# Performance work log

Hardware: AMD Instinct MI355X
Metric: run time of the kernel (lower is better)

## Reference

```python
import jax, jax.numpy as jnp
import numpy as np

B, CK, H, W = 1, 64, 30, 54
O, CV, M = 3, 512, 32400
TOP_K = 20


def setup_inputs() -> dict:
    key = jax.random.key(0)
    k1, k2, k3 = jax.random.split(key, 3)
    return {
        "qk": jax.random.normal(k1, (B, CK, H, W), dtype=jnp.float32),
        "mem_k": jax.random.normal(k2, (1, CK, M), dtype=jnp.float32),
        "mem_v": jax.random.normal(k3, (O, CV, M), dtype=jnp.float32),
        "top_k": TOP_K,
    }


def _softmax_w_top(aff, top_k):
    # aff: [B, M, Q]; top-k softmax over the memory axis M (dim=1), zeros elsewhere.
    b, m, q = aff.shape
    xt = aff.transpose(0, 2, 1)                      # [B, Q, M] -> top_k over last axis
    vals, idx = jax.lax.top_k(xt, top_k)             # [B, Q, K]
    soft = jax.nn.softmax(vals, axis=-1)             # stable softmax over the K kept entries
    w = jnp.zeros_like(xt).at[
        jnp.arange(b)[:, None, None],
        jnp.arange(q)[None, :, None],
        idx,
    ].set(soft)                                      # scatter back into [B, Q, M]
    return w.transpose(0, 2, 1)                      # [B, M, Q]


def reference(qk, mem_k, mem_v, top_k):
    b, ck, h, w = qk.shape
    q = h * w
    qk2 = qk.reshape(b, ck, q)                       # [B, CK, Q]
    mk = mem_k[0]                                    # [CK, M]
    a_sq = jnp.sum(mk * mk, axis=0)                  # [M]
    ab = jnp.einsum("cm,bcq->bmq", mk, qk2)          # [B, M, Q]
    scale = np.sqrt(ck).astype(np.float32)
    affinity = (2.0 * ab - a_sq[None, :, None]) / scale
    weights = _softmax_w_top(affinity, top_k)        # [B, M, Q] sparse (top_k nonzeros per column)
    readout = jnp.einsum("ocm,bmq->obcq", mem_v, weights)  # [O, B, CV, Q]
    o, _, cv, _ = readout.shape
    return readout.reshape(o, b, cv, h, q // h)      # [O, B, CV, H, W]
```

## Files before the change

### kernel.cpp

```cpp
#include <hip/hip_runtime.h>
#include <math.h>

#define M_TOT   32400
#define CKDIM   64
#define QTOT    1620
#define QPAD    1792
#define OCDIM   1536
#define TOPK    20
#define NSPLIT  45
#define MSPLIT  720
#define NCHUNK  15
#define KSPLIT  20
#define KEYSQ   (NSPLIT*KSPLIT)
#define POOL    32

typedef __attribute__((ext_vector_type(8))) short bf16x8;
typedef __attribute__((ext_vector_type(4))) float f32x4;

__device__ __forceinline__ float bf2f(unsigned short u) {
    union { unsigned int i; float f; } v;
    v.i = ((unsigned int)u) << 16;
    return v.f;
}

__device__ __forceinline__ unsigned short f2bf(float f) {
    union { float f; unsigned int i; } u;
    u.f = f;
    unsigned int r = u.i + 0x7FFF + ((u.i >> 16) & 1);
    return (unsigned short)(r >> 16);
}

__device__ __forceinline__ float med3f(float a, float b, float c) {
#if __has_builtin(__builtin_amdgcn_fmed3f)
    return __builtin_amdgcn_fmed3f(a, b, c);
#else
    return fmaxf(fminf(a, b), fminf(fmaxf(a, b), c));
#endif
}

#define INS5(t, x) do {                    \
    t[4] = med3f((x), t[3], t[4]);         \
    t[3] = med3f((x), t[2], t[3]);         \
    t[2] = med3f((x), t[1], t[2]);         \
    t[1] = med3f((x), t[0], t[1]);         \
    t[0] = fmaxf(t[0], (x));               \
} while (0)

#define INS8(t, x) do {                    \
    t[7] = med3f((x), t[6], t[7]);         \
    t[6] = med3f((x), t[5], t[6]);         \
    t[5] = med3f((x), t[4], t[5]);         \
    t[4] = med3f((x), t[3], t[4]);         \
    t[3] = med3f((x), t[2], t[3]);         \
    t[2] = med3f((x), t[1], t[2]);         \
    t[1] = med3f((x), t[0], t[1]);         \
    t[0] = fmaxf(t[0], (x));               \
} while (0)

__global__ __launch_bounds__(256) void k_cast(const float* __restrict__ mk,
                                              const float* __restrict__ qk,
                                              unsigned short* __restrict__ mkT,
                                              unsigned short* __restrict__ qkT) {
    int idx = blockIdx.x * 256 + threadIdx.x;
    if (idx < M_TOT) {
        int m = idx;
        uint4* dst = (uint4*)(mkT + (size_t)m * CKDIM);
        #pragma unroll
        for (int g = 0; g < CKDIM / 8; ++g) {
            unsigned int r[4];
            #pragma unroll
            for (int p = 0; p < 4; ++p) {
                float v0 = mk[(size_t)(g * 8 + p * 2 + 0) * M_TOT + m];
                float v1 = mk[(size_t)(g * 8 + p * 2 + 1) * M_TOT + m];
                r[p] = (unsigned int)f2bf(v0) | ((unsigned int)f2bf(v1) << 16);
            }
            dst[g] = make_uint4(r[0], r[1], r[2], r[3]);
        }
    } else if (idx < M_TOT + QPAD) {
        int q = idx - M_TOT;
        uint4* dst = (uint4*)(qkT + (size_t)q * CKDIM);
        #pragma unroll
        for (int g = 0; g < CKDIM / 8; ++g) {
            unsigned int r[4];
            #pragma unroll
            for (int p = 0; p < 4; ++p) {
                float v0 = (q < QTOT) ? qk[(size_t)(g * 8 + p * 2 + 0) * QTOT + q] : 0.f;
                float v1 = (q < QTOT) ? qk[(size_t)(g * 8 + p * 2 + 1) * QTOT + q] : 0.f;
                r[p] = (unsigned int)f2bf(v0) | ((unsigned int)f2bf(v1) << 16);
            }
            dst[g] = make_uint4(r[0], r[1], r[2], r[3]);
        }
    }
}

__global__ __launch_bounds__(256) void k_asq(const float* __restrict__ mk,
                                             float* __restrict__ asq) {
    int m = blockIdx.x * 256 + threadIdx.x;
    if (m >= M_TOT) return;
    float s = 0.f;
    #pragma unroll
    for (int c = 0; c < CKDIM; ++c) { float v = mk[(size_t)c * M_TOT + m]; s += v * v; }
    asq[m] = s;
}

__global__ __launch_bounds__(64) void k_topk_mfma(const unsigned short* __restrict__ mkT,
                                                  const unsigned short* __restrict__ qkT,
                                                  const float* __restrict__ asq,
                                                  float* __restrict__ pkeys) {
    const int lane = threadIdx.x;
    const int l15  = lane & 15;
    const int quad = lane >> 4;
    const int q_base = blockIdx.x * 64;
    const int sp     = blockIdx.y;
    const int m_base = sp * MSPLIT;

    bf16x8 bF[4][2];
    #pragma unroll
    for (int qt = 0; qt < 4; ++qt) {
        const unsigned short* p = qkT + (size_t)(q_base + qt * 16 + l15) * CKDIM + quad * 8;
        bF[qt][0] = *(const bf16x8*)(p);
        bF[qt][1] = *(const bf16x8*)(p + 32);
    }

    float key5[4][5];
    #pragma unroll
    for (int qt = 0; qt < 4; ++qt)
        #pragma unroll
        for (int j = 0; j < 5; ++j) key5[qt][j] = -INFINITY;

    for (int ch = 0; ch < NCHUNK; ++ch) {
        #pragma unroll
        for (int mt = 0; mt < 3; ++mt) {
            const int mrow = m_base + ch * 48 + mt * 16;
            f32x4 aq = *(const f32x4*)(asq + mrow + quad * 4);
            f32x4 cinit = -0.5f * aq;
            const unsigned short* pa = mkT + (size_t)(mrow + l15) * CKDIM + quad * 8;
            bf16x8 aF0 = *(const bf16x8*)(pa);
            bf16x8 aF1 = *(const bf16x8*)(pa + 32);
            const unsigned int mq = (unsigned int)(mrow + quad * 4);
            #pragma unroll
            for (int qt = 0; qt < 4; ++qt) {
                f32x4 c = cinit;
                c = __builtin_amdgcn_mfma_f32_16x16x32_bf16(aF0, bF[qt][0], c, 0, 0, 0);
                c = __builtin_amdgcn_mfma_f32_16x16x32_bf16(aF1, bF[qt][1], c, 0, 0, 0);
                #pragma unroll
                for (int i = 0; i < 4; ++i) {
                    unsigned int kb = (__float_as_uint(c[i]) & 0xFFFF8000u) | (mq + i);
                    float kf = __uint_as_float(kb);
                    INS5(key5[qt], kf);
                }
            }
        }
    }

    #pragma unroll
    for (int qt = 0; qt < 4; ++qt) {
        const int q = q_base + qt * 16 + l15;
        float* dst = pkeys + (size_t)q * KEYSQ + sp * KSPLIT + quad * 5;
        #pragma unroll
        for (int j = 0; j < 5; ++j) dst[j] = key5[qt][j];
    }
}

__global__ __launch_bounds__(64) void k_select(const float* __restrict__ pkeys,
                                               const float* __restrict__ mk,
                                               const float* __restrict__ qk,
                                               const float* __restrict__ asq,
                                               uint2* __restrict__ qw) {
    const int q    = blockIdx.x;
    const int lane = threadIdx.x;

    float t[8];
    #pragma unroll
    for (int j = 0; j < 8; ++j) t[j] = -INFINITY;
    const float* src = pkeys + (size_t)q * KEYSQ;
    #pragma unroll
    for (int i = 0; i < 15; ++i) {
        int s = lane + i * 64;
        float v = (s < KEYSQ) ? src[s] : -INFINITY;
        INS8(t, v);
    }

    float mykey = -INFINITY;
    for (int r = 0; r < POOL; ++r) {
        float h = t[0];
        float wm = h;
        #pragma unroll
        for (int off = 32; off; off >>= 1) wm = fmaxf(wm, __shfl_xor(wm, off));
        bool win = (h == wm);
        t[0] = win ? t[1] : t[0];
        t[1] = win ? t[2] : t[1];
        t[2] = win ? t[3] : t[2];
        t[3] = win ? t[4] : t[3];
        t[4] = win ? t[5] : t[4];
        t[5] = win ? t[6] : t[5];
        t[6] = win ? t[7] : t[6];
        t[7] = win ? -INFINITY : t[7];
        if (lane == r) mykey = wm;
    }

    const int  m_l = (int)(__float_as_uint(mykey) & 0x7FFFu);
    const bool act = (lane < POOL);

    float dot = 0.f;
    #pragma unroll
    for (int c = 0; c < CKDIM; ++c)
        dot += mk[(size_t)c * M_TOT + m_l] * qk[(size_t)c * QTOT + q];
    float aff = act ? (2.f * dot - asq[m_l]) * 0.125f : -INFINITY;

    __shared__ float kv[TOPK];
    __shared__ int   ki[TOPK];

    for (int r = 0; r < TOPK; ++r) {
        float bv = aff;
        int   bm = m_l;
        #pragma unroll
        for (int off = 32; off; off >>= 1) {
            float ov = __shfl_xor(bv, off);
            int   om = __shfl_xor(bm, off);
            if (ov > bv || (ov == bv && om < bm)) { bv = ov; bm = om; }
        }
        if (aff == bv && m_l == bm) aff = -INFINITY;
        if (lane == 0) { kv[r] = bv; ki[r] = bm; }
    }
    __syncthreads();

    float e = (lane < TOPK) ? __expf(kv[lane] - kv[0]) : 0.f;
    float sum = e;
    #pragma unroll
    for (int off = 32; off; off >>= 1) sum += __shfl_xor(sum, off);

    if (lane < TOPK) {
        unsigned int wbits;
        { union { float f; unsigned int i; } u; u.f = e / sum; wbits = u.i; }
        qw[(size_t)q * TOPK + lane] = make_uint2((unsigned int)ki[lane], wbits);
    }
}

__global__ __launch_bounds__(512, 4) void k_readout(const float* __restrict__ mv,
                                                    const uint2* __restrict__ qw,
                                                    float* __restrict__ out) {
    __shared__ unsigned short row[M_TOT];
    const int oc  = blockIdx.x;
    const int tid = threadIdx.x;

    const uint4* s4 = (const uint4*)(mv + (size_t)oc * M_TOT);
    uint4 tmp[15];
    #pragma unroll
    for (int it = 0; it < 15; ++it) tmp[it] = s4[tid + it * 512];
    uint4 tail;
    const int ti_idx = 15 * 512 + tid;
    if (tid < M_TOT / 4 - 15 * 512)
        tail = s4[ti_idx];

    ushort4* d4 = (ushort4*)row;
    #pragma unroll
    for (int it = 0; it < 15; ++it) {
        uint4 v = tmp[it];
        ushort4 h;
        h.x = f2bf(__uint_as_float(v.x));
        h.y = f2bf(__uint_as_float(v.y));
        h.z = f2bf(__uint_as_float(v.z));
        h.w = f2bf(__uint_as_float(v.w));
        d4[tid + it * 512] = h;
    }
    if (tid < M_TOT / 4 - 15 * 512) {
        ushort4 h;
        h.x = f2bf(__uint_as_float(tail.x));
        h.y = f2bf(__uint_as_float(tail.y));
        h.z = f2bf(__uint_as_float(tail.z));
        h.w = f2bf(__uint_as_float(tail.w));
        d4[ti_idx] = h;
    }
    __syncthreads();

    #pragma unroll
    for (int j = 0; j < 4; ++j) {
        int q = tid + j * 512;
        if (q >= QTOT) break;
        const uint2* p = qw + (size_t)q * TOPK;
        float acc = 0.f;
        #pragma unroll
        for (int k = 0; k < TOPK; ++k) {
            uint2 e = p[k];
            acc += __uint_as_float(e.y) * bf2f(row[e.x]);
        }
        out[(size_t)oc * QTOT + q] = acc;
    }
}

extern "C" void kernel_launch(void* const* d_in, const int* in_sizes, int n_in,
                              void* d_out, int out_size, void* d_ws, size_t ws_size,
                              hipStream_t stream) {
    const float* qk = (const float*)d_in[0];
    const float* mk = (const float*)d_in[1];
    const float* mv = (const float*)d_in[2];
    float* out = (float*)d_out;

    char* ws = (char*)d_ws;
    float*          asq   = (float*)(ws);
    unsigned short* qkT   = (unsigned short*)(ws + 131072);
    unsigned short* mkT   = (unsigned short*)(ws + 360448);
    float*          pkeys = (float*)(ws + 4507648);
    uint2*          qw    = (uint2*)(ws + 10958848);

    k_cast     <<<dim3((M_TOT + QPAD + 255) / 256), dim3(256), 0, stream>>>(mk, qk, mkT, qkT);
    k_asq      <<<dim3((M_TOT + 255) / 256),        dim3(256), 0, stream>>>(mk, asq);
    k_topk_mfma<<<dim3(28, NSPLIT),                 dim3(64),  0, stream>>>(mkT, qkT, asq, pkeys);
    k_select   <<<dim3(QTOT),                       dim3(64),  0, stream>>>(pkeys, mk, qk, asq, qw);
    k_readout  <<<dim3(OCDIM),                      dim3(512), 0, stream>>>(mv, qw, out);
}
```

Measured before the change: 387.5 us.

## Fuse cast and key-norm kernels, add fp32 transposed keys, prefetch weights in readout

Merges the bf16 cast and squared-norm kernels into one prep kernel that reads memory keys once and also writes fp32 row-major copies of keys and queries. The select kernel then rescores candidates with contiguous float4 loads instead of strided column gathers. The readout kernel splits its value-row staging into two phases and prefetches the first query's top-k entries early so that load overlaps the conversion. The cost is an extra ~8MB of fp32 transposed writes in the prep kernel and higher register pressure in readout.

```diff
diff --git a/kernel.cpp b/kernel.cpp
--- a/kernel.cpp
+++ b/kernel.cpp
@@ -57,50 +57,59 @@
     t[0] = fmaxf(t[0], (x));               \
 } while (0)
 
-__global__ __launch_bounds__(256) void k_cast(const float* __restrict__ mk,
+__global__ __launch_bounds__(256) void k_prep(const float* __restrict__ mk,
                                               const float* __restrict__ qk,
+                                              float* __restrict__ asq,
                                               unsigned short* __restrict__ mkT,
-                                              unsigned short* __restrict__ qkT) {
+                                              float* __restrict__ mkTf,
+                                              unsigned short* __restrict__ qkT,
+                                              float* __restrict__ qkTf) {
     int idx = blockIdx.x * 256 + threadIdx.x;
     if (idx < M_TOT) {
-        int m = idx;
-        uint4* dst = (uint4*)(mkT + (size_t)m * CKDIM);
-        #pragma unroll
-        for (int g = 0; g < CKDIM / 8; ++g) {
+        const int m = idx;
+        float vals[CKDIM];
+        float s = 0.f;
+        #pragma unroll
+        for (int c = 0; c < CKDIM; ++c) {
+            vals[c] = mk[(size_t)c * M_TOT + m];
+            s += vals[c] * vals[c];
+        }
+        asq[m] = s;
+        uint4* db = (uint4*)(mkT + (size_t)m * CKDIM);
+        #pragma unroll
+        for (int g = 0; g < 8; ++g) {
             unsigned int r[4];
             #pragma unroll
-            for (int p = 0; p < 4; ++p) {
-                float v0 = mk[(size_t)(g * 8 + p * 2 + 0) * M_TOT + m];
-                float v1 = mk[(size_t)(g * 8 + p * 2 + 1) * M_TOT + m];
-                r[p] = (unsigned int)f2bf(v0) | ((unsigned int)f2bf(v1) << 16);
-            }
-            dst[g] = make_uint4(r[0], r[1], r[2], r[3]);
-        }
+            for (int p = 0; p < 4; ++p)
+                r[p] = (unsigned int)f2bf(vals[g * 8 + 2 * p])
+                     | ((unsigned int)f2bf(vals[g * 8 + 2 * p + 1]) << 16);
+            db[g] = make_uint4(r[0], r[1], r[2], r[3]);
+        }
+        float4* df = (float4*)(mkTf + (size_t)m * CKDIM);
+        #pragma unroll
+        for (int g = 0; g < 16; ++g)
+            df[g] = make_float4(vals[4 * g], vals[4 * g + 1], vals[4 * g + 2], vals[4 * g + 3]);
     } else if (idx < M_TOT + QPAD) {
-        int q = idx - M_TOT;
-        uint4* dst = (uint4*)(qkT + (size_t)q * CKDIM);
-        #pragma unroll
-        for (int g = 0; g < CKDIM / 8; ++g) {
+        const int q = idx - M_TOT;
+        float vals[CKDIM];
+        #pragma unroll
+        for (int c = 0; c < CKDIM; ++c)
+            vals[c] = (q < QTOT) ? qk[(size_t)c * QTOT + q] : 0.f;
+        uint4* db = (uint4*)(qkT + (size_t)q * CKDIM);
+        #pragma unroll
+        for (int g = 0; g < 8; ++g) {
             unsigned int r[4];
             #pragma unroll
-            for (int p = 0; p < 4; ++p) {
-                float v0 = (q < QTOT) ? qk[(size_t)(g * 8 + p * 2 + 0) * QTOT + q] : 0.f;
-                float v1 = (q < QTOT) ? qk[(size_t)(g * 8 + p * 2 + 1) * QTOT + q] : 0.f;
-                r[p] = (unsigned int)f2bf(v0) | ((unsigned int)f2bf(v1) << 16);
-            }
-            dst[g] = make_uint4(r[0], r[1], r[2], r[3]);
-        }
-    }
-}
-
-__global__ __launch_bounds__(256) void k_asq(const float* __restrict__ mk,
-                                             float* __restrict__ asq) {
-    int m = blockIdx.x * 256 + threadIdx.x;
-    if (m >= M_TOT) return;
-    float s = 0.f;
-    #pragma unroll
-    for (int c = 0; c < CKDIM; ++c) { float v = mk[(size_t)c * M_TOT + m]; s += v * v; }
-    asq[m] = s;
+            for (int p = 0; p < 4; ++p)
+                r[p] = (unsigned int)f2bf(vals[g * 8 + 2 * p])
+                     | ((unsigned int)f2bf(vals[g * 8 + 2 * p + 1]) << 16);
+            db[g] = make_uint4(r[0], r[1], r[2], r[3]);
+        }
+        float4* df = (float4*)(qkTf + (size_t)q * CKDIM);
+        #pragma unroll
+        for (int g = 0; g < 16; ++g)
+            df[g] = make_float4(vals[4 * g], vals[4 * g + 1], vals[4 * g + 2], vals[4 * g + 3]);
+    }
 }
 
 __global__ __launch_bounds__(64) void k_topk_mfma(const unsigned short* __restrict__ mkT,
@@ -163,8 +172,8 @@
 }
 
 __global__ __launch_bounds__(64) void k_select(const float* __restrict__ pkeys,
-                                               const float* __restrict__ mk,
-                                               const float* __restrict__ qk,
+                                               const float* __restrict__ mkTf,
+                                               const float* __restrict__ qkTf,
                                                const float* __restrict__ asq,
                                                uint2* __restrict__ qw) {
     const int q    = blockIdx.x;
@@ -202,10 +211,15 @@
     const int  m_l = (int)(__float_as_uint(mykey) & 0x7FFFu);
     const bool act = (lane < POOL);
 
+    const float4* rm = (const float4*)(mkTf + (size_t)m_l * CKDIM);
+    const float4* rq = (const float4*)(qkTf + (size_t)q * CKDIM);
     float dot = 0.f;
     #pragma unroll
-    for (int c = 0; c < CKDIM; ++c)
-        dot += mk[(size_t)c * M_TOT + m_l] * qk[(size_t)c * QTOT + q];
+    for (int g = 0; g < 16; ++g) {
+        float4 a = rm[g];
+        float4 b = rq[g];
+        dot += a.x * b.x + a.y * b.y + a.z * b.z + a.w * b.w;
+    }
     float aff = act ? (2.f * dot - asq[m_l]) * 0.125f : -INFINITY;
 
     __shared__ float kv[TOPK];
@@ -245,24 +259,47 @@
     const int tid = threadIdx.x;
 
     const uint4* s4 = (const uint4*)(mv + (size_t)oc * M_TOT);
-    uint4 tmp[15];
-    #pragma unroll
-    for (int it = 0; it < 15; ++it) tmp[it] = s4[tid + it * 512];
-    uint4 tail;
-    const int ti_idx = 15 * 512 + tid;
-    if (tid < M_TOT / 4 - 15 * 512)
-        tail = s4[ti_idx];
-
     ushort4* d4 = (ushort4*)row;
-    #pragma unroll
-    for (int it = 0; it < 15; ++it) {
-        uint4 v = tmp[it];
+
+    uint4 tA[8];
+    #pragma unroll
+    for (int it = 0; it < 8; ++it) tA[it] = s4[tid + it * 512];
+
+    uint2 e0[TOPK];
+    {
+        const uint2* p0 = qw + (size_t)tid * TOPK;
+        #pragma unroll
+        for (int k = 0; k < TOPK; ++k) e0[k] = p0[k];
+    }
+
+    #pragma unroll
+    for (int it = 0; it < 8; ++it) {
+        uint4 v = tA[it];
         ushort4 h;
         h.x = f2bf(__uint_as_float(v.x));
         h.y = f2bf(__uint_as_float(v.y));
         h.z = f2bf(__uint_as_float(v.z));
         h.w = f2bf(__uint_as_float(v.w));
         d4[tid + it * 512] = h;
+    }
+
+    uint4 tB[7];
+    #pragma unroll
+    for (int it = 0; it < 7; ++it) tB[it] = s4[tid + (8 + it) * 512];
+    uint4 tail;
+    const int ti_idx = 15 * 512 + tid;
+    if (tid < M_TOT / 4 - 15 * 512)
+        tail = s4[ti_idx];
+
+    #pragma unroll
+    for (int it = 0; it < 7; ++it) {
+        uint4 v = tB[it];
+        ushort4 h;
+        h.x = f2bf(__uint_as_float(v.x));
+        h.y = f2bf(__uint_as_float(v.y));
+        h.z = f2bf(__uint_as_float(v.z));
+        h.w = f2bf(__uint_as_float(v.w));
+        d4[tid + (8 + it) * 512] = h;
     }
     if (tid < M_TOT / 4 - 15 * 512) {
         ushort4 h;
@@ -274,8 +311,15 @@
     }
     __syncthreads();
 
-    #pragma unroll
-    for (int j = 0; j < 4; ++j) {
+    {
+        float acc = 0.f;
+        #pragma unroll
+        for (int k = 0; k < TOPK; ++k)
+            acc += __uint_as_float(e0[k].y) * bf2f(row[e0[k].x]);
+        out[(size_t)oc * QTOT + tid] = acc;
+    }
+    #pragma unroll
+    for (int j = 1; j < 4; ++j) {
         int q = tid + j * 512;
         if (q >= QTOT) break;
         const uint2* p = qw + (size_t)q * TOPK;
@@ -301,12 +345,14 @@
     float*          asq   = (float*)(ws);
     unsigned short* qkT   = (unsigned short*)(ws + 131072);
     unsigned short* mkT   = (unsigned short*)(ws + 360448);
-    float*          pkeys = (float*)(ws + 4507648);
-    uint2*          qw    = (uint2*)(ws + 10958848);
-
-    k_cast     <<<dim3((M_TOT + QPAD + 255) / 256), dim3(256), 0, stream>>>(mk, qk, mkT, qkT);
-    k_asq      <<<dim3((M_TOT + 255) / 256),        dim3(256), 0, stream>>>(mk, asq);
+    float*          mkTf  = (float*)(ws + 4507648);
+    float*          qkTf  = (float*)(ws + 12802048);
+    float*          pkeys = (float*)(ws + 13260800);
+    uint2*          qw    = (uint2*)(ws + 19712000);
+
+    k_prep     <<<dim3((M_TOT + QPAD + 255) / 256), dim3(256), 0, stream>>>(
+                   mk, qk, asq, mkT, mkTf, qkT, qkTf);
     k_topk_mfma<<<dim3(28, NSPLIT),                 dim3(64),  0, stream>>>(mkT, qkT, asq, pkeys);
-    k_select   <<<dim3(QTOT),                       dim3(64),  0, stream>>>(pkeys, mk, qk, asq, qw);
+    k_select   <<<dim3(QTOT),                       dim3(64),  0, stream>>>(pkeys, mkTf, qkTf, asq, qw);
     k_readout  <<<dim3(OCDIM),                      dim3(512), 0, stream>>>(mv, qw, out);
 }
```

Result: faster. 369.9 us (-4.5%).
